# Performance work log

Hardware: AMD Instinct MI355X
Metric: run time of the kernel (lower is better)

## Reference

```python
import jax, jax.numpy as jnp
import numpy as np

B, S, D = 2, 2048, 2048
VOCAB = 32000
CUTOFFS = [1000, 2000, 5000, VOCAB]  # torch appends vocab_size
N_CLUSTERS = 3
HEAD_SIZE = CUTOFFS[0] + N_CLUSTERS  # 1003
LN_EPS = 1e-5
INIT = 0.02


def setup_inputs() -> dict:
    key = jax.random.key(0)
    ks = jax.random.split(key, 10)
    inp = {
        "x": jax.random.normal(ks[0], (B, S, D), dtype=jnp.float32),
        "targets": jax.random.randint(ks[1], (B, S), 0, VOCAB, dtype=jnp.int32),
        "gamma": jnp.ones((D,), jnp.float32),
        "beta": jnp.zeros((D,), jnp.float32),
        "head_w": jax.random.normal(ks[2], (HEAD_SIZE, D), jnp.float32) * INIT,
    }
    # tail clusters: hsz = D // 4**i, osz = cutoffs[i] - cutoffs[i-1]
    for i in range(1, 4):
        hsz = D // (4 ** i)
        osz = CUTOFFS[i] - CUTOFFS[i - 1]
        inp[f"t{i}_w1"] = jax.random.normal(ks[2 + 2 * i], (hsz, D), jnp.float32) * INIT
        inp[f"t{i}_w2"] = jax.random.normal(ks[3 + 2 * i], (osz, hsz), jnp.float32) * INIT
    return inp


def reference(x, targets, gamma, beta, head_w, t1_w1, t1_w2, t2_w1, t2_w2, t3_w1, t3_w2):
    # LayerNorm over last dim
    mu = jnp.mean(x, axis=-1, keepdims=True)
    var = jnp.mean(jnp.square(x - mu), axis=-1, keepdims=True)
    xn = (x - mu) * jax.lax.rsqrt(var + LN_EPS) * gamma + beta

    # shift: predict token t+1 from hidden t
    h = xn[:, :-1, :].reshape(-1, x.shape[-1])      # [N, D]
    lbl = targets[:, 1:].reshape(-1)                # [N]
    n = h.shape[0]
    rows = jnp.arange(n)

    # head: shortlist (first cutoff) + one logit per tail cluster
    head_lp = jax.nn.log_softmax(h @ head_w.T, axis=-1)  # [N, 1003]
    out = head_lp[rows, jnp.clip(lbl, 0, CUTOFFS[0] - 1)]

    tails = [(t1_w1, t1_w2), (t2_w1, t2_w2), (t3_w1, t3_w2)]
    for i, (w1, w2) in enumerate(tails):
        low, high = CUTOFFS[i], CUTOFFS[i + 1]
        tail_lp = jax.nn.log_softmax((h @ w1.T) @ w2.T, axis=-1)  # [N, osz]
        rel = jnp.clip(lbl - low, 0, high - low - 1)
        lp = head_lp[:, CUTOFFS[0] + i] + tail_lp[rows, rel]
        out = jnp.where((lbl >= low) & (lbl < high), lp, out)

    return -jnp.mean(out)  # NLL loss, matches .loss of AdaptiveLogSoftmaxWithLoss
```

## Files before the change

kernel.cpp:

```cpp
#include <hip/hip_runtime.h>
#include <hip/hip_bf16.h>
#include <math.h>

#define BB 2
#define SS 2048
#define DD 2048
#define NR (BB*(SS-1))
#define NRP 4096
#define MT_LD 768
#define MT_P2 512
#define MT_P3 640

#define L2E 1.4426950408889634f
#define LN2F 0.6931471805599453f
#define LSE_SHIFT 4.0f
#define LSE_NC (-LSE_SHIFT * L2E)
#define WSCALE 16.0f
#define WINV   0.0625f

typedef short  bh8   __attribute__((ext_vector_type(8)));
typedef float  f32x4 __attribute__((ext_vector_type(4)));
typedef long   l64x2 __attribute__((ext_vector_type(2)));

__device__ inline float bfl(unsigned short b) { return __uint_as_float(((unsigned)b) << 16); }
__device__ inline float expsh(float v) { return __builtin_amdgcn_exp2f(fmaf(v, L2E, LSE_NC)); }

__device__ inline float block_sum256(float v) {
    __shared__ float tmp[4];
    #pragma unroll
    for (int o = 32; o > 0; o >>= 1) v += __shfl_down(v, o, 64);
    int lane = threadIdx.x & 63, w = threadIdx.x >> 6;
    if (lane == 0) tmp[w] = v;
    __syncthreads();
    float r = tmp[0] + tmp[1] + tmp[2] + tmp[3];
    __syncthreads();
    return r;
}

__device__ inline unsigned pack_fp8x4(float a, float b, float c, float d) {
    unsigned r = 0;
    r = __builtin_amdgcn_cvt_pk_fp8_f32(a, b, r, false);
    r = __builtin_amdgcn_cvt_pk_fp8_f32(c, d, r, true);
    return r;
}

struct CastSegs {
    const float* src[7];
    void* dst[7];
    int n_src[7];
    int n_tot[7];
    int b0[7];
    int isfp8[7];
    float scl[7];
};
struct AParams {
    const float* x; const float* gamma; const float* beta;
    unsigned char* h8;
    CastSegs sg; int castBlocks;
    const int* targets;
    int *relH;
    int *cnt;
    int *rlist1, *rlist2, *rlist3;
    int *cidx1, *cidx2, *cidx3;
    int *rel1c, *rel2c, *rel3c;
    float *S0, *S1c, *S2c, *out;
};

__global__ __launch_bounds__(256) void stageA(AParams p) {
    int blk = blockIdx.x, tid = threadIdx.x;
    if (blk < NRP) {
        int n = blk;
        unsigned char* hr = p.h8 + (size_t)n * DD;
        if (n >= NR) { *(uint2*)(hr + tid * 8) = make_uint2(0,0); return; }
        int b = n / (SS - 1), t = n % (SS - 1);
        const float4* xr = (const float4*)(p.x + (size_t)(b * SS + t) * DD);
        float4 a = xr[tid * 2];
        float4 c = xr[tid * 2 + 1];
        float sum = a.x + a.y + a.z + a.w + c.x + c.y + c.z + c.w;
        sum = block_sum256(sum);
        float mu = sum * (1.0f / DD);
        float d[8] = {a.x-mu, a.y-mu, a.z-mu, a.w-mu, c.x-mu, c.y-mu, c.z-mu, c.w-mu};
        float sq = 0.f;
        #pragma unroll
        for (int i = 0; i < 8; ++i) sq += d[i] * d[i];
        sq = block_sum256(sq);
        float rstd = rsqrtf(sq * (1.0f / DD) + 1e-5f);
        const float4* g4 = (const float4*)p.gamma;
        const float4* be4 = (const float4*)p.beta;
        float4 g1 = g4[tid*2], g2 = g4[tid*2+1];
        float4 b1 = be4[tid*2], b2 = be4[tid*2+1];
        float gg[8] = {g1.x,g1.y,g1.z,g1.w,g2.x,g2.y,g2.z,g2.w};
        float bb[8] = {b1.x,b1.y,b1.z,b1.w,b2.x,b2.y,b2.z,b2.w};
        float o[8];
        #pragma unroll
        for (int i = 0; i < 8; ++i) o[i] = d[i] * rstd * gg[i] + bb[i];
        uint2 pk;
        pk.x = pack_fp8x4(o[0], o[1], o[2], o[3]);
        pk.y = pack_fp8x4(o[4], o[5], o[6], o[7]);
        *(uint2*)(hr + tid * 8) = pk;
        return;
    }
    blk -= NRP;
    if (blk < p.castBlocks) {
        int k = 0;
        #pragma unroll
        for (int i = 1; i < 7; ++i) if (blk >= p.sg.b0[i]) k = i;
        int i4 = (blk - p.sg.b0[k]) * 1024 + tid * 4;
        if (i4 >= p.sg.n_tot[k]) return;
        float4 v = make_float4(0.f,0.f,0.f,0.f);
        if (i4 < p.sg.n_src[k]) v = *(const float4*)(p.sg.src[k] + i4);
        if (p.sg.isfp8[k]) {
            unsigned pk = pack_fp8x4(v.x * WSCALE, v.y * WSCALE, v.z * WSCALE, v.w * WSCALE);
            *(unsigned*)((unsigned char*)p.sg.dst[k] + i4) = pk;
        } else {
            float sc = p.sg.scl[k];
            __align__(8) __hip_bfloat16 o[4] = {
                __float2bfloat16(v.x * sc), __float2bfloat16(v.y * sc),
                __float2bfloat16(v.z * sc), __float2bfloat16(v.w * sc)};
            *(uint2*)((__hip_bfloat16*)p.sg.dst[k] + i4) = *(uint2*)o;
        }
        return;
    }
    blk -= p.castBlocks;
    int n = blk * 256 + tid;
    if (n >= NRP) return;
    int lbl = -1;
    if (n < NR) {
        int b = n / (SS - 1), t = n % (SS - 1);
        lbl = p.targets[b * SS + t + 1];
    }
    bool v = n < NR;
    p.relH[n] = v ? (lbl < 1000 ? lbl : 999) : -1;
    if (v) {
        if (lbl >= 1000 && lbl < 2000) {
            int ci = atomicAdd(&p.cnt[0], 1);
            p.rlist1[ci] = n; p.cidx1[n] = ci;
            int r1 = lbl - 1000; p.rel1c[ci] = r1 > 999 ? 999 : r1;
        } else if (lbl >= 2000 && lbl < 5000) {
            int ci = atomicAdd(&p.cnt[1], 1);
            p.rlist2[ci] = n; p.cidx2[n] = ci;
            int r2 = lbl - 2000; p.rel2c[ci] = r2 > 2999 ? 2999 : r2;
        } else if (lbl >= 5000) {
            int ci = atomicAdd(&p.cnt[2], 1);
            p.rlist3[ci] = n; p.cidx3[n] = ci;
            int r3 = lbl - 5000; p.rel3c[ci] = r3 > 26999 ? 26999 : r3;
        }
    }
    p.S0[n] = 0.f; p.S1c[n] = 0.f; p.S2c[n] = 0.f;
    if (n == 0) p.out[0] = 0.f;
}

__global__ __launch_bounds__(256) void megaF(
        const unsigned char* __restrict__ A,
        const unsigned char* __restrict__ W,
        __hip_bfloat16* __restrict__ megaT,
        const int* __restrict__ relH,
        float* __restrict__ S0, float* __restrict__ aux) {
    __shared__ __align__(16) unsigned char smF[2][12288];
    int tid = threadIdx.x, wv = tid >> 6, lane = tid & 63;
    int row0 = blockIdx.y * 64, col0 = blockIdx.x * 128;
    int wrow = (wv >> 1) * 32, wcol = (wv & 1) * 64;
    f32x4 acc[2][4];
    #pragma unroll
    for (int i = 0; i < 2; ++i)
        #pragma unroll
        for (int j = 0; j < 4; ++j) acc[i][j] = (f32x4){0.f,0.f,0.f,0.f};
    int sr = lane >> 2;
    int kp = (((lane & 3) ^ (sr & 3)) * 16);
    int mrow = lane & 15;
    int qx = (((lane >> 4) ^ (lane & 3)) * 16);

    auto stage = [&](int buf, int k0) {
        {
            int r = wv * 16 + sr;
            const void* ga = A + (size_t)(row0 + r) * DD + k0 + kp;
            void* la = (char*)&smF[buf][0] + wv * 1024 + lane * 16;
            __builtin_amdgcn_global_load_lds(
                (const __attribute__((address_space(1))) void*)ga,
                (__attribute__((address_space(3))) void*)la, 16, 0, 0);
        }
        #pragma unroll
        for (int i = 0; i < 2; ++i) {
            int chunk = wv * 2 + i;
            int r = chunk * 16 + sr;
            const void* gw = W + (size_t)(col0 + r) * DD + k0 + kp;
            void* lw = (char*)&smF[buf][4096] + chunk * 1024 + lane * 16;
            __builtin_amdgcn_global_load_lds(
                (const __attribute__((address_space(1))) void*)gw,
                (__attribute__((address_space(3))) void*)lw, 16, 0, 0);
        }
    };

    stage(0, 0);
    asm volatile("s_waitcnt vmcnt(0)" ::: "memory");
    __builtin_amdgcn_s_barrier();
    __builtin_amdgcn_sched_barrier(0);
    int cur = 0;
    for (int k0 = 0; k0 < DD; k0 += 64) {
        if (k0 + 64 < DD) stage(cur ^ 1, k0 + 64);
        const unsigned char* As = &smF[cur][0];
        const unsigned char* Ws = &smF[cur][4096];
        l64x2 af[2], bfr[4];
        #pragma unroll
        for (int t = 0; t < 2; ++t)
            af[t]  = *(const l64x2*)(As + (wrow + t*16 + mrow) * 64 + qx);
        #pragma unroll
        for (int t = 0; t < 4; ++t)
            bfr[t] = *(const l64x2*)(Ws + (wcol + t*16 + mrow) * 64 + qx);
        #pragma unroll
        for (int s = 0; s < 2; ++s)
            #pragma unroll
            for (int i = 0; i < 2; ++i)
                #pragma unroll
                for (int j = 0; j < 4; ++j)
                    acc[i][j] = __builtin_amdgcn_mfma_f32_16x16x32_fp8_fp8(
                        af[i][s], bfr[j][s], acc[i][j], 0, 0, 0);
        asm volatile("s_waitcnt vmcnt(0) lgkmcnt(0)" ::: "memory");
        __builtin_amdgcn_s_barrier();
        __builtin_amdgcn_sched_barrier(0);
        cur ^= 1;
    }
    int ccol = lane & 15, g = lane >> 4;
    if (blockIdx.x < 8) {
        int grs[2][4], rh[2][4];
        float ps[2][4];
        #pragma unroll
        for (int i = 0; i < 2; ++i)
            #pragma unroll
            for (int r = 0; r < 4; ++r) {
                grs[i][r] = row0 + wrow + i*16 + g*4 + r;
                rh[i][r] = relH[grs[i][r]];
                ps[i][r] = 0.f;
            }
        #pragma unroll
        for (int i = 0; i < 2; ++i)
            #pragma unroll
            for (int j = 0; j < 4; ++j) {
                int gc = col0 + wcol + j*16 + ccol;
                bool inr = gc < 1003;
                #pragma unroll
                for (int r = 0; r < 4; ++r) {
                    float v = acc[i][j][r] * WINV;
                    if (gc == rh[i][r]) aux[grs[i][r]*8 + 0] = v;
                    if (gc >= 1000 && gc < 1003) aux[grs[i][r]*8 + 2 + (gc - 1000)] = v;
                    ps[i][r] += inr ? expsh(v) : 0.f;
                }
            }
        #pragma unroll
        for (int off = 1; off < 16; off <<= 1)
            #pragma unroll
            for (int i = 0; i < 2; ++i)
                #pragma unroll
                for (int r = 0; r < 4; ++r) ps[i][r] += __shfl_xor(ps[i][r], off, 64);
        if (ccol == 0)
            #pragma unroll
            for (int i = 0; i < 2; ++i)
                #pragma unroll
                for (int r = 0; r < 4; ++r) atomicAdd(&S0[grs[i][r]], ps[i][r]);
    } else {
        int cb = col0 - 1024 + wcol;
        #pragma unroll
        for (int i = 0; i < 2; ++i) {
            size_t gr0 = row0 + wrow + i*16 + g*4;
            #pragma unroll
            for (int j = 0; j < 4; ++j) {
                size_t gc = cb + j*16 + ccol;
                #pragma unroll
                for (int r = 0; r < 4; ++r)
                    megaT[(gr0 + r) * MT_LD + gc] = __float2bfloat16(acc[i][j][r] * WINV);
            }
        }
    }
}

__device__ void tail_gemm(const __hip_bfloat16* A, int lda,
        const __hip_bfloat16* W, int K, int bx, int by, int validCols,
        const int* relc, float* S, float* tgt, char* sm,
        const int* rlist, int nrows) {
    __hip_bfloat16* As = (__hip_bfloat16*)sm;
    __hip_bfloat16* Ws = (__hip_bfloat16*)(sm + 4096);
    int tid = threadIdx.x, wv = tid >> 6, lane = tid & 63;
    int row0 = by * 64, col0 = bx * 128;
    int wrow = (wv >> 1) * 32, wcol = (wv & 1) * 64;
    f32x4 acc[2][4];
    #pragma unroll
    for (int i = 0; i < 2; ++i)
        #pragma unroll
        for (int j = 0; j < 4; ++j) acc[i][j] = (f32x4){0.f,0.f,0.f,0.f};
    int sr = lane >> 2;
    int sk = (((lane & 3) ^ (sr & 3)) * 8);
    int mrow = lane & 15;
    int qx = (((lane >> 4) ^ (lane & 3)) * 16);

    const __hip_bfloat16* gA[3];
    #pragma unroll
    for (int i = 0; i < 3; ++i) {
        int c = wv * 3 + i;
        if (c < 4) {
            int r = row0 + c * 16 + sr;
            int orow = rlist[r < nrows ? r : nrows - 1];
            gA[i] = A + (size_t)orow * lda + sk;
        } else gA[i] = nullptr;
    }

    for (int k0 = 0; k0 < K; k0 += 32) {
        __syncthreads();
        #pragma unroll
        for (int i = 0; i < 3; ++i) {
            int c = wv * 3 + i;
            const __hip_bfloat16* gsrc;
            char* ldst;
            if (c < 4) {
                gsrc = gA[i] + k0;
                ldst = (char*)As + c * 1024 + lane * 16;
            } else {
                int cw = c - 4;
                gsrc = W + (size_t)(col0 + cw * 16 + sr) * K + k0 + sk;
                ldst = (char*)Ws + cw * 1024 + lane * 16;
            }
            __builtin_amdgcn_global_load_lds(
                (const __attribute__((address_space(1))) void*)gsrc,
                (__attribute__((address_space(3))) void*)ldst, 16, 0, 0);
        }
        __syncthreads();
        bh8 af[2], bfr[4];
        #pragma unroll
        for (int t = 0; t < 2; ++t)
            af[t] = *(const bh8*)((const char*)As + (wrow + t*16 + mrow) * 64 + qx);
        #pragma unroll
        for (int t = 0; t < 4; ++t)
            bfr[t] = *(const bh8*)((const char*)Ws + (wcol + t*16 + mrow) * 64 + qx);
        #pragma unroll
        for (int i = 0; i < 2; ++i)
            #pragma unroll
            for (int j = 0; j < 4; ++j)
                acc[i][j] = __builtin_amdgcn_mfma_f32_16x16x32_bf16(af[i], bfr[j], acc[i][j], 0, 0, 0);
    }
    int ccol = lane & 15, g = lane >> 4;
    int grs[2][4], rh[2][4];
    float p[2][4];
    #pragma unroll
    for (int i = 0; i < 2; ++i)
        #pragma unroll
        for (int r = 0; r < 4; ++r) {
            grs[i][r] = row0 + wrow + i*16 + g*4 + r;
            rh[i][r] = relc[grs[i][r] < nrows ? grs[i][r] : 0];
            p[i][r] = 0.f;
        }
    #pragma unroll
    for (int i = 0; i < 2; ++i)
        #pragma unroll
        for (int j = 0; j < 4; ++j) {
            int gc = col0 + wcol + j*16 + ccol;
            bool inr = gc < validCols;
            #pragma unroll
            for (int r = 0; r < 4; ++r) {
                float v = acc[i][j][r];
                if (gc == rh[i][r] && grs[i][r] < nrows) tgt[grs[i][r]] = v;
                p[i][r] += inr ? expsh(v) : 0.f;
            }
        }
    #pragma unroll
    for (int off = 1; off < 16; off <<= 1)
        #pragma unroll
        for (int i = 0; i < 2; ++i)
            #pragma unroll
            for (int r = 0; r < 4; ++r) p[i][r] += __shfl_xor(p[i][r], off, 64);
    if (ccol == 0)
        #pragma unroll
        for (int i = 0; i < 2; ++i)
            #pragma unroll
            for (int r = 0; r < 4; ++r)
                if (grs[i][r] < nrows) atomicAdd(&S[grs[i][r]], p[i][r]);
}

#define T3_TILES 1688
#define T3_SPLIT 16
#define T3_TPC   106
__device__ void t3_partial_body(const __hip_bfloat16* megaT,
        const __hip_bfloat16* w2b, float* pS, const int* rlist3, int n3,
        int idx, int tid, float* red ) {
    int rg = idx >> 4, cs = idx & 15;
    int wv = tid >> 6, lane = tid & 63;
    int q = lane >> 4, cm = lane & 15;
    int row0 = rg * 64;
    bh8 af[4];
    #pragma unroll
    for (int h = 0; h < 4; ++h) {
        int r = row0 + h*16 + cm;
        int orow = rlist3[r < n3 ? r : n3 - 1];
        af[h] = *(const bh8*)(megaT + (size_t)orow * MT_LD + MT_P3 + q * 8);
    }
    int tile0 = cs * T3_TPC;
    int tile1 = tile0 + T3_TPC; if (tile1 > T3_TILES) tile1 = T3_TILES;
    float s[4][4];
    #pragma unroll
    for (int h = 0; h < 4; ++h)
        #pragma unroll
        for (int r = 0; r < 4; ++r) s[h][r] = 0.f;
    int ot = tile0 + wv;
    auto baddr = [&](int t) {
        int tc = t < tile1 ? t : tile1 - 1;
        return (const bh8*)(w2b + (size_t)(tc * 16 + cm) * 32 + q * 8);
    };
    bh8 p0 = *baddr(ot), p1 = *baddr(ot + 4), p2 = *baddr(ot + 8), p3 = *baddr(ot + 12);
    for (; ot < tile1; ot += 4) {
        bh8 bcur = p0;
        p0 = p1; p1 = p2; p2 = p3;
        int otn = ot + 16;
        if (otn < tile1)
            p3 = *(const bh8*)(w2b + (size_t)(otn * 16 + cm) * 32 + q * 8);
        f32x4 c[4];
        #pragma unroll
        for (int h = 0; h < 4; ++h)
            c[h] = __builtin_amdgcn_mfma_f32_16x16x32_bf16(af[h], bcur, (f32x4){0,0,0,0}, 0, 0, 0);
        #pragma unroll
        for (int h = 0; h < 4; ++h)
            #pragma unroll
            for (int r = 0; r < 4; ++r) s[h][r] += __builtin_amdgcn_exp2f(c[h][r]);
    }
    #pragma unroll
    for (int off = 1; off < 16; off <<= 1)
        #pragma unroll
        for (int h = 0; h < 4; ++h)
            #pragma unroll
            for (int r = 0; r < 4; ++r) s[h][r] += __shfl_xor(s[h][r], off, 64);
    if (cm == 0)
        #pragma unroll
        for (int h = 0; h < 4; ++h)
            #pragma unroll
            for (int r = 0; r < 4; ++r)
                red[wv * 64 + h*16 + q*4 + r] = s[h][r];
    __syncthreads();
    if (tid < 64)
        pS[(size_t)(row0 + tid) * T3_SPLIT + cs] =
            red[tid] + red[64 + tid] + red[128 + tid] + red[192 + tid];
}

__device__ void t3_gather_body(const __hip_bfloat16* megaT, const __hip_bfloat16* w2b,
        const int* rlist3, const int* rel3c, int n3, float* tt2c, int idx, int tid) {
    int ci = idx * 256 + tid;
    if (ci >= n3) return;
    int orow = rlist3[ci];
    int rc = rel3c[ci];
    const unsigned short* pa = (const unsigned short*)(megaT + (size_t)orow * MT_LD + MT_P3);
    const unsigned short* pw = (const unsigned short*)(w2b + (size_t)rc * 32);
    float acc = 0.f;
    #pragma unroll
    for (int k = 0; k < 32; ++k) acc += bfl(pa[k]) * bfl(pw[k]);
    tt2c[ci] = acc;
}

#define NT3 (64 * T3_SPLIT)
#define NT1 512
#define NT2 1536
#define NGATH 16
__global__ __launch_bounds__(256) void fatC(const __hip_bfloat16* __restrict__ megaT,
        const __hip_bfloat16* __restrict__ t1w2b, const __hip_bfloat16* __restrict__ t2w2b,
        const __hip_bfloat16* __restrict__ w2b3,
        const int* __restrict__ cnt,
        const int* __restrict__ rlist1, const int* __restrict__ rlist2, const int* __restrict__ rlist3,
        const int* __restrict__ rel1c, const int* __restrict__ rel2c, const int* __restrict__ rel3c,
        float* __restrict__ S1c, float* __restrict__ S2c, float* __restrict__ pS3,
        float* __restrict__ tt0c, float* __restrict__ tt1c, float* __restrict__ tt2c) {
    __shared__ __align__(16) char sm[12288];
    int idx = blockIdx.x, tid = threadIdx.x;
    if (idx < NT3) {
        int n3 = cnt[2];
        if ((idx >> 4) * 64 >= n3) return;
        t3_partial_body(megaT, w2b3, pS3, rlist3, n3, idx, tid, (float*)sm);
        return;
    }
    idx -= NT3;
    if (idx < NT1) {
        int n1 = cnt[0];
        int by = idx / 8, bx = idx % 8;
        if (by * 64 >= n1) return;
        tail_gemm(megaT, MT_LD, t1w2b, 512, bx, by, 1000, rel1c, S1c, tt0c, sm, rlist1, n1);
        return;
    }
    idx -= NT1;
    if (idx < NT2) {
        int n2 = cnt[1];
        int by = idx / 24, bx = idx % 24;
        if (by * 64 >= n2) return;
        tail_gemm(megaT + MT_P2, MT_LD, t2w2b, 128, bx, by, 3000, rel2c, S2c, tt1c, sm, rlist2, n2);
        return;
    }
    idx -= NT2;
    t3_gather_body(megaT, w2b3, rlist3, rel3c, cnt[2], tt2c, idx, tid);
}

__global__ __launch_bounds__(256) void final_kernel(const float* __restrict__ aux,
        const int* __restrict__ targets,
        const float* __restrict__ S0, const float* __restrict__ S1c, const float* __restrict__ S2c,
        const float* __restrict__ pS3,
        const float* __restrict__ tt0c, const float* __restrict__ tt1c, const float* __restrict__ tt2c,
        const int* __restrict__ cidx1, const int* __restrict__ cidx2, const int* __restrict__ cidx3,
        float* __restrict__ out) {
    int n = blockIdx.x * 256 + threadIdx.x;
    float local = 0.f;
    if (n < NR) {
        int b = n / (SS - 1), t = n % (SS - 1);
        int lbl = targets[b * SS + t + 1];
        float lse = logf(S0[n]) + LSE_SHIFT;
        float o;
        if (lbl < 1000)      o = aux[n*8 + 0] - lse;
        else if (lbl < 2000) {
            int ci = cidx1[n];
            o = (aux[n*8 + 2] - lse) + (tt0c[ci] - (logf(S1c[ci]) + LSE_SHIFT));
        } else if (lbl < 5000) {
            int ci = cidx2[n];
            o = (aux[n*8 + 3] - lse) + (tt1c[ci] - (logf(S2c[ci]) + LSE_SHIFT));
        } else {
            int ci = cidx3[n];
            float S3 = 0.f;
            const float4* p4 = (const float4*)(pS3 + (size_t)ci * T3_SPLIT);
            #pragma unroll
            for (int c = 0; c < T3_SPLIT/4; ++c) {
                float4 v = p4[c];
                S3 += v.x + v.y + v.z + v.w;
            }
            S3 -= 8.0f;
            o = (aux[n*8 + 4] - lse) + (tt2c[ci] * LN2F - logf(S3));
        }
        local = o;
    }
    local = block_sum256(local);
    if (threadIdx.x == 0) atomicAdd(out, -local / (float)NR);
}

extern "C" void kernel_launch(void* const* d_in, const int* in_sizes, int n_in,
                              void* d_out, int out_size, void* d_ws, size_t ws_size,
                              hipStream_t stream) {
    const float* x      = (const float*)d_in[0];
    const int*   targets= (const int*)d_in[1];
    const float* gamma  = (const float*)d_in[2];
    const float* beta   = (const float*)d_in[3];
    const float* head_w = (const float*)d_in[4];
    const float* t1_w1  = (const float*)d_in[5];
    const float* t1_w2  = (const float*)d_in[6];
    const float* t2_w1  = (const float*)d_in[7];
    const float* t2_w2  = (const float*)d_in[8];
    const float* t3_w1  = (const float*)d_in[9];
    const float* t3_w2  = (const float*)d_in[10];
    (void)in_sizes; (void)n_in; (void)out_size; (void)ws_size;

    char* base = (char*)d_ws;
    size_t off = 0;
    auto ab = [&](size_t nbytes) { char* p = base + off; off += (nbytes + 15) & ~(size_t)15; return p; };
    unsigned char* h8     = (unsigned char*)ab((size_t)NRP * DD);
    unsigned char* w1cat8 = (unsigned char*)ab((size_t)1792 * DD);
    __hip_bfloat16* megaT = (__hip_bfloat16*)ab((size_t)NRP * MT_LD * 2);
    __hip_bfloat16* t1w2b = (__hip_bfloat16*)ab((size_t)1024 * 512 * 2);
    __hip_bfloat16* t2w2b = (__hip_bfloat16*)ab((size_t)3072 * 128 * 2);
    __hip_bfloat16* w2b3  = (__hip_bfloat16*)ab((size_t)27008 * 32 * 2);
    float* aux = (float*)ab((size_t)NRP * 8 * 4);
    float* pS3 = (float*)ab((size_t)NRP * T3_SPLIT * 4);
    float* S0  = (float*)ab(NRP * 4);
    float* S1c = (float*)ab(NRP * 4);
    float* S2c = (float*)ab(NRP * 4);
    int* relH  = (int*)ab(NRP * 4);
    int* cnt   = (int*)ab(4 * 4);
    int* rlist1= (int*)ab(NRP * 4);
    int* rlist2= (int*)ab(NRP * 4);
    int* rlist3= (int*)ab(NRP * 4);
    int* cidx1 = (int*)ab(NRP * 4);
    int* cidx2 = (int*)ab(NRP * 4);
    int* cidx3 = (int*)ab(NRP * 4);
    int* rel1c = (int*)ab(NRP * 4);
    int* rel2c = (int*)ab(NRP * 4);
    int* rel3c = (int*)ab(NRP * 4);
    float* tt0c= (float*)ab(NRP * 4);
    float* tt1c= (float*)ab(NRP * 4);
    float* tt2c= (float*)ab(NRP * 4);

    hipMemsetAsync(cnt, 0, 4 * 4, stream);

    AParams p;
    p.x = x; p.gamma = gamma; p.beta = beta; p.h8 = h8;
    p.targets = targets;
    p.relH = relH;
    p.cnt = cnt;
    p.rlist1 = rlist1; p.rlist2 = rlist2; p.rlist3 = rlist3;
    p.cidx1 = cidx1; p.cidx2 = cidx2; p.cidx3 = cidx3;
    p.rel1c = rel1c; p.rel2c = rel2c; p.rel3c = rel3c;
    p.S0 = S0; p.S1c = S1c; p.S2c = S2c; p.out = (float*)d_out;
    const float* srcs[7] = {head_w, t1_w1, t2_w1, t3_w1, t1_w2, t2_w2, t3_w2};
    void* dsts[7] = {w1cat8, w1cat8 + (size_t)1024*2048, w1cat8 + (size_t)1536*2048,
                     w1cat8 + (size_t)1664*2048, t1w2b, t2w2b, w2b3};
    int nsrc[7] = {1003*2048, 512*2048, 128*2048, 32*2048, 1000*512, 3000*128, 27000*32};
    int ntot[7] = {1024*2048, 512*2048, 128*2048, 128*2048, 1024*512, 3072*128, 27008*32};
    int isf8[7] = {1, 1, 1, 1, 0, 0, 0};
    float scls[7] = {1.f, 1.f, 1.f, 1.f, 1.0f, 1.0f, L2E};
    int blk = 0;
    for (int i = 0; i < 7; ++i) {
        p.sg.src[i] = srcs[i]; p.sg.dst[i] = dsts[i];
        p.sg.n_src[i] = nsrc[i]; p.sg.n_tot[i] = ntot[i];
        p.sg.isfp8[i] = isf8[i];
        p.sg.scl[i] = scls[i];
        p.sg.b0[i] = blk;
        blk += (ntot[i] + 1023) / 1024;
    }
    p.castBlocks = blk;

    stageA<<<NRP + blk + 16, 256, 0, stream>>>(p);
    megaF<<<dim3(14, 64), 256, 0, stream>>>(h8, w1cat8, megaT, relH, S0, aux);
    fatC<<<NT3 + NT1 + NT2 + NGATH, 256, 0, stream>>>(megaT, t1w2b, t2w2b, w2b3,
            cnt, rlist1, rlist2, rlist3, rel1c, rel2c, rel3c,
            S1c, S2c, pS3, tt0c, tt1c, tt2c);
    final_kernel<<<16, 256, 0, stream>>>(aux, targets, S0, S1c, S2c, pS3,
            tt0c, tt1c, tt2c, cidx1, cidx2, cidx3, (float*)d_out);
}
```

Before: 176.1 us.

## Compute tail-1/2 projections only for gathered cluster rows in megaF

```diff
diff --git a/kernel.cpp b/kernel.cpp
--- a/kernel.cpp
+++ b/kernel.cpp
@@ -155,10 +155,16 @@
         const unsigned char* __restrict__ W,
         __hip_bfloat16* __restrict__ megaT,
         const int* __restrict__ relH,
+        const int* __restrict__ cnt,
+        const int* __restrict__ rlist1, const int* __restrict__ rlist2,
         float* __restrict__ S0, float* __restrict__ aux) {
     __shared__ __align__(16) unsigned char smF[2][12288];
     int tid = threadIdx.x, wv = tid >> 6, lane = tid & 63;
-    int row0 = blockIdx.y * 64, col0 = blockIdx.x * 128;
+    int bx = blockIdx.x;
+    int row0 = blockIdx.y * 64, col0 = bx * 128;
+    const int* rl = nullptr; int nrow = NRP;
+    if (bx >= 8 && bx < 12) { rl = rlist1; nrow = cnt[0]; if (row0 >= nrow) return; }
+    else if (bx == 12)      { rl = rlist2; nrow = cnt[1]; if (row0 >= nrow) return; }
     int wrow = (wv >> 1) * 32, wcol = (wv & 1) * 64;
     f32x4 acc[2][4];
     #pragma unroll
@@ -170,13 +176,15 @@
     int mrow = lane & 15;
     int qx = (((lane >> 4) ^ (lane & 3)) * 16);
 
+    int ar = row0 + wv * 16 + sr;
+    int orow = rl ? rl[ar < nrow ? ar : nrow - 1] : ar;
+    const unsigned char* gabase = A + (size_t)orow * DD + kp;
+
     auto stage = [&](int buf, int k0) {
         {
-            int r = wv * 16 + sr;
-            const void* ga = A + (size_t)(row0 + r) * DD + k0 + kp;
             void* la = (char*)&smF[buf][0] + wv * 1024 + lane * 16;
             __builtin_amdgcn_global_load_lds(
-                (const __attribute__((address_space(1))) void*)ga,
+                (const __attribute__((address_space(1))) void*)(gabase + k0),
                 (__attribute__((address_space(3))) void*)la, 16, 0, 0);
         }
         #pragma unroll
@@ -221,7 +229,7 @@
         cur ^= 1;
     }
     int ccol = lane & 15, g = lane >> 4;
-    if (blockIdx.x < 8) {
+    if (bx < 8) {
         int grs[2][4], rh[2][4];
         float ps[2][4];
         #pragma unroll
@@ -275,8 +283,7 @@
 
 __device__ void tail_gemm(const __hip_bfloat16* A, int lda,
         const __hip_bfloat16* W, int K, int bx, int by, int validCols,
-        const int* relc, float* S, float* tgt, char* sm,
-        const int* rlist, int nrows) {
+        const int* relc, float* S, float* tgt, char* sm, int nrows) {
     __hip_bfloat16* As = (__hip_bfloat16*)sm;
     __hip_bfloat16* Ws = (__hip_bfloat16*)(sm + 4096);
     int tid = threadIdx.x, wv = tid >> 6, lane = tid & 63;
@@ -292,17 +299,6 @@
     int mrow = lane & 15;
     int qx = (((lane >> 4) ^ (lane & 3)) * 16);
 
-    const __hip_bfloat16* gA[3];
-    #pragma unroll
-    for (int i = 0; i < 3; ++i) {
-        int c = wv * 3 + i;
-        if (c < 4) {
-            int r = row0 + c * 16 + sr;
-            int orow = rlist[r < nrows ? r : nrows - 1];
-            gA[i] = A + (size_t)orow * lda + sk;
-        } else gA[i] = nullptr;
-    }
-
     for (int k0 = 0; k0 < K; k0 += 32) {
         __syncthreads();
         #pragma unroll
@@ -311,7 +307,7 @@
             const __hip_bfloat16* gsrc;
             char* ldst;
             if (c < 4) {
-                gsrc = gA[i] + k0;
+                gsrc = A + (size_t)(row0 + c * 16 + sr) * lda + k0 + sk;
                 ldst = (char*)As + c * 1024 + lane * 16;
             } else {
                 int cw = c - 4;
@@ -344,7 +340,7 @@
         #pragma unroll
         for (int r = 0; r < 4; ++r) {
             grs[i][r] = row0 + wrow + i*16 + g*4 + r;
-            rh[i][r] = relc[grs[i][r] < nrows ? grs[i][r] : 0];
+            rh[i][r] = grs[i][r] < nrows ? relc[grs[i][r]] : 0;
             p[i][r] = 0.f;
         }
     #pragma unroll
@@ -459,7 +455,7 @@
         const __hip_bfloat16* __restrict__ t1w2b, const __hip_bfloat16* __restrict__ t2w2b,
         const __hip_bfloat16* __restrict__ w2b3,
         const int* __restrict__ cnt,
-        const int* __restrict__ rlist1, const int* __restrict__ rlist2, const int* __restrict__ rlist3,
+        const int* __restrict__ rlist3,
         const int* __restrict__ rel1c, const int* __restrict__ rel2c, const int* __restrict__ rel3c,
         float* __restrict__ S1c, float* __restrict__ S2c, float* __restrict__ pS3,
         float* __restrict__ tt0c, float* __restrict__ tt1c, float* __restrict__ tt2c) {
@@ -476,7 +472,7 @@
         int n1 = cnt[0];
         int by = idx / 8, bx = idx % 8;
         if (by * 64 >= n1) return;
-        tail_gemm(megaT, MT_LD, t1w2b, 512, bx, by, 1000, rel1c, S1c, tt0c, sm, rlist1, n1);
+        tail_gemm(megaT, MT_LD, t1w2b, 512, bx, by, 1000, rel1c, S1c, tt0c, sm, n1);
         return;
     }
     idx -= NT1;
@@ -484,7 +480,7 @@
         int n2 = cnt[1];
         int by = idx / 24, bx = idx % 24;
         if (by * 64 >= n2) return;
-        tail_gemm(megaT + MT_P2, MT_LD, t2w2b, 128, bx, by, 3000, rel2c, S2c, tt1c, sm, rlist2, n2);
+        tail_gemm(megaT + MT_P2, MT_LD, t2w2b, 128, bx, by, 3000, rel2c, S2c, tt1c, sm, n2);
         return;
     }
     idx -= NT2;
@@ -605,9 +601,9 @@
     p.castBlocks = blk;
 
     stageA<<<NRP + blk + 16, 256, 0, stream>>>(p);
-    megaF<<<dim3(14, 64), 256, 0, stream>>>(h8, w1cat8, megaT, relH, S0, aux);
+    megaF<<<dim3(14, 64), 256, 0, stream>>>(h8, w1cat8, megaT, relH, cnt, rlist1, rlist2, S0, aux);
     fatC<<<NT3 + NT1 + NT2 + NGATH, 256, 0, stream>>>(megaT, t1w2b, t2w2b, w2b3,
-            cnt, rlist1, rlist2, rlist3, rel1c, rel2c, rel3c,
+            cnt, rlist3, rel1c, rel2c, rel3c,
             S1c, S2c, pS3, tt0c, tt1c, tt2c);
     final_kernel<<<16, 256, 0, stream>>>(aux, targets, S0, S1c, S2c, pS3,
             tt0c, tt1c, tt2c, cidx1, cidx2, cidx3, (float*)d_out);
```

Measured after the change: 170.0 us. 3.4% less time.
